# Performance work log

Measured on AMD Instinct MI355X. Metric: run time of the kernel, lower is better.

The kernel has to match this reference:

```python
import jax, jax.numpy as jnp
import numpy as np

UNITS = 20
EPS_GPE_STN = 0.1


def _w_lateral(units=UNITS, eps=EPS_GPE_STN):
    # Faithful port of generate_distance_matrix: grid_size = int(sqrt(units))
    grid_size = int(units ** 0.5)
    idx = np.arange(units)
    xi, yi = np.divmod(idx, grid_size)
    d = (xi[:, None] - xi[None, :]) ** 2 + (yi[:, None] - yi[None, :]) ** 2
    return jnp.asarray(np.exp(-d.astype(np.float32) / eps), dtype=jnp.float32)


def setup_inputs() -> dict:
    key = jax.random.key(0)
    ks = jax.random.split(key, 8)
    B = 524288
    k = 1.0 / np.sqrt(UNITS)  # PyTorch LSTMCell init scale
    x = jax.random.normal(ks[0], (B, UNITS), dtype=jnp.float32)
    h = jax.random.normal(ks[1], (B, UNITS), dtype=jnp.float32)
    c = jax.random.normal(ks[2], (B, UNITS), dtype=jnp.float32)
    W_ih = jax.random.uniform(ks[3], (4 * UNITS, UNITS), jnp.float32, -k, k)
    W_hh = jax.random.uniform(ks[4], (4 * UNITS, UNITS), jnp.float32, -k, k)
    b_ih = jax.random.uniform(ks[5], (4 * UNITS,), jnp.float32, -k, k)
    b_hh = jax.random.uniform(ks[6], (4 * UNITS,), jnp.float32, -k, k)
    W_lat = _w_lateral()
    return {"x": x, "h": h, "c": c, "W_ih": W_ih, "W_hh": W_hh,
            "b_ih": b_ih, "b_hh": b_hh, "W_lat": W_lat}


def reference(x, h, c, W_ih, W_hh, b_ih, b_hh, W_lat):
    # nn.LSTMCell: gates in (i, f, g, o) order
    gates = x @ W_ih.T + h @ W_hh.T + (b_ih + b_hh)  # [B, 4U]
    i, f, g, o = jnp.split(gates, 4, axis=-1)
    c_next = jax.nn.sigmoid(f) * c + jax.nn.sigmoid(i) * jnp.tanh(g)
    h_lstm = jax.nn.sigmoid(o) * jnp.tanh(c_next)
    # bmm(W_lateral, h[:, :, None]).squeeze(-1) == h @ W_lat.T, then tanh
    h_next = jnp.tanh(h_lstm @ W_lat.T)
    return (h_next, c_next)
```

## Files before the change

kernel.cpp:

```cpp
#include <hip/hip_runtime.h>

#define UNITS 20

typedef __attribute__((ext_vector_type(8))) short short8;
typedef __attribute__((ext_vector_type(4))) float floatx4;
typedef unsigned int u32;
typedef unsigned short u16;

__device__ __forceinline__ float rcpf_fast(float x) { return __builtin_amdgcn_rcpf(x); }
__device__ __forceinline__ float sigmoidf_fast(float x) { return rcpf_fast(1.0f + __expf(-x)); }
__device__ __forceinline__ float tanhf_fast(float x) { return 1.0f - 2.0f * rcpf_fast(1.0f + __expf(2.0f * x)); }

__device__ __forceinline__ u32 f2bf(float f) {
  u32 u = __builtin_bit_cast(u32, f);
  u += 0x7fffu + ((u >> 16) & 1u);
  return u >> 16;
}
__device__ __forceinline__ u32 pack2(float a, float b) { return f2bf(a) | (f2bf(b) << 16); }

__global__ void prep_kernel(const float* __restrict__ W_ih, const float* __restrict__ W_hh,
                            const float* __restrict__ b_ih, const float* __restrict__ b_hh,
                            const float* __restrict__ W_lat,
                            u16* __restrict__ fragsG, u16* __restrict__ fragsL,
                            float4* __restrict__ bias4) {
  int tid = threadIdx.x;
  for (int e = tid; e < 768; e += 256) {
    int fi = e >> 6, lane = e & 63;
    int r = lane & 15, q = lane >> 4;
    short8 v8;
    if (fi < 10) {
      int t = fi >> 1, cc = fi & 1;
      int gr = (r & 3) * 20 + (r >> 2) * 5 + t;
#pragma unroll
      for (int j = 0; j < 8; ++j) {
        int k = cc * 32 + q * 8 + j;
        float v = 0.0f;
        if (k < 20) v = W_ih[gr * UNITS + k];
        else if (k < 40) v = W_hh[gr * UNITS + (k - 20)];
        v8[j] = (short)f2bf(v);
      }
      *(short8*)(fragsG + (size_t)e * 8) = v8;
    } else {
      int t = fi - 10;
      int vr = t * 16 + r;
#pragma unroll
      for (int j = 0; j < 8; ++j) {
        int k = q * 8 + j;
        float v = (vr < 20 && k < 20) ? W_lat[vr * UNITS + k] : 0.0f;
        v8[j] = (short)f2bf(v);
      }
      *(short8*)(fragsL + (size_t)(t * 64 + lane) * 8) = v8;
    }
  }
  if (tid < 20)
    bias4[tid] = make_float4(b_ih[tid] + b_hh[tid],
                             b_ih[20 + tid] + b_hh[20 + tid],
                             b_ih[40 + tid] + b_hh[40 + tid],
                             b_ih[60 + tid] + b_hh[60 + tid]);
}

#define SZE 72
#define SHL 40

__global__ __launch_bounds__(256) void stn_main(
    const float* __restrict__ x, const float* __restrict__ h, const float* __restrict__ c,
    const u16* __restrict__ fragsG, const u16* __restrict__ fragsL,
    const float4* __restrict__ bias4, float* __restrict__ out, int B) {
  __shared__ unsigned char smem[19456];
  u16*   Zs = (u16*)smem;
  float* Cn = (float*)smem;
  float* Cs = (float*)(smem + 9216);
  float* Hn = (float*)(smem + 9216);
  u16*   Hl = (u16*)(smem + 14336);

  const int tid  = threadIdx.x;
  const int lane = tid & 63;
  const int wv   = tid >> 6;
  const int m = lane & 15, q = lane >> 4;
  const long rowBase = (long)blockIdx.x * 64;
  const int  myrow = wv * 16 + m;
  const long f4base = rowBase * 5;
  const long f4max = (long)B * 5 - 1;

  {
    const float4* x4 = (const float4*)x;
    const float4* h4 = (const float4*)h;
    const float4* c4 = (const float4*)c;
    for (int e = tid; e < 320; e += 256) {
      long gi = f4base + e; if (gi > f4max) gi = f4max;
      int row = e / 5, part = e - row * 5;
      float4 vx = x4[gi];
      u32* zp = (u32*)(Zs + row * SZE + part * 4);
      zp[0] = pack2(vx.x, vx.y); zp[1] = pack2(vx.z, vx.w);
      float4 vh = h4[gi];
      u32* zq = (u32*)(Zs + row * SZE + 20 + part * 4);
      zq[0] = pack2(vh.x, vh.y); zq[1] = pack2(vh.z, vh.w);
      ((float4*)Cs)[e] = c4[gi];
    }
    int r = tid & 63, s = tid >> 6;
    u32* zp = (u32*)(Zs + r * SZE + 40);
    zp[s * 3 + 0] = 0; zp[s * 3 + 1] = 0; zp[s * 3 + 2] = 0;
    u32* hp = (u32*)(Hl + r * SHL + 20);
    hp[s] = 0; if (s < 2) hp[s + 4] = 0;
  }
  __syncthreads();

  short8 bfr[2];
#pragma unroll
  for (int cc = 0; cc < 2; ++cc)
    bfr[cc] = *(const short8*)(Zs + myrow * SZE + cc * 32 + q * 8);

  floatx4 acc[5];
#pragma unroll
  for (int t = 0; t < 5; ++t) {
    float4 b4 = bias4[q * 5 + t];
    acc[t] = (floatx4){b4.x, b4.y, b4.z, b4.w};
#pragma unroll
    for (int cc = 0; cc < 2; ++cc) {
      short8 af = *(const short8*)(fragsG + (size_t)((t * 2 + cc) * 64 + lane) * 8);
      acc[t] = __builtin_amdgcn_mfma_f32_16x16x32_bf16(af, bfr[cc], acc[t], 0, 0, 0);
    }
  }

  float cnv[5];
#pragma unroll
  for (int t = 0; t < 5; ++t) {
    int u = q * 5 + t;
    float ig = sigmoidf_fast(acc[t][0]);
    float fg = sigmoidf_fast(acc[t][1]);
    float gg = tanhf_fast(acc[t][2]);
    float og = sigmoidf_fast(acc[t][3]);
    float cv = Cs[myrow * 20 + u];
    float cn = fg * cv + ig * gg;
    cnv[t] = cn;
    Hl[myrow * SHL + u] = (u16)f2bf(og * tanhf_fast(cn));
  }
  __syncthreads();

  short8 bl = *(const short8*)(Hl + myrow * SHL + q * 8);
  floatx4 accL[2];
#pragma unroll
  for (int t = 0; t < 2; ++t) {
    short8 al = *(const short8*)(fragsL + (size_t)(t * 64 + lane) * 8);
    accL[t] = __builtin_amdgcn_mfma_f32_16x16x32_bf16(al, bl, (floatx4){0.f, 0.f, 0.f, 0.f}, 0, 0, 0);
  }

#pragma unroll
  for (int t = 0; t < 5; ++t) Cn[myrow * 20 + q * 5 + t] = cnv[t];
#pragma unroll
  for (int t = 0; t < 2; ++t)
#pragma unroll
    for (int reg = 0; reg < 4; ++reg) {
      int v = t * 16 + q * 4 + reg;
      if (v < 20) Hn[myrow * 20 + v] = tanhf_fast(accL[t][reg]);
    }
  __syncthreads();

  {
    float4* outh4 = (float4*)out;
    float4* outc4 = (float4*)(out + (size_t)B * UNITS);
    for (int e = tid; e < 320; e += 256) {
      long gi = f4base + e;
      if (gi <= f4max) {
        outh4[gi] = ((const float4*)Hn)[e];
        outc4[gi] = ((const float4*)Cn)[e];
      }
    }
  }
}

extern "C" void kernel_launch(void* const* d_in, const int* in_sizes, int n_in,
                              void* d_out, int out_size, void* d_ws, size_t ws_size,
                              hipStream_t stream) {
  const float* x     = (const float*)d_in[0];
  const float* h     = (const float*)d_in[1];
  const float* c     = (const float*)d_in[2];
  const float* W_ih  = (const float*)d_in[3];
  const float* W_hh  = (const float*)d_in[4];
  const float* b_ih  = (const float*)d_in[5];
  const float* b_hh  = (const float*)d_in[6];
  const float* W_lat = (const float*)d_in[7];
  float* out = (float*)d_out;

  u16*    fragsG = (u16*)d_ws;
  u16*    fragsL = (u16*)((char*)d_ws + 10240);
  float4* bias4  = (float4*)((char*)d_ws + 12288);

  int B = in_sizes[0] / UNITS;
  prep_kernel<<<1, 256, 0, stream>>>(W_ih, W_hh, b_ih, b_hh, W_lat, fragsG, fragsL, bias4);
  int grid = (B + 63) / 64;
  stn_main<<<grid, 256, 0, stream>>>(x, h, c, fragsG, fragsL, bias4, out, B);
}
```

Measured before the change: 204.9 us.

## Load LSTM inputs straight into MFMA fragments with a persistent grid-stride loop

Removes the LDS staging of x, h and c and of the c_next and h_next outputs. Each lane now loads its own float4 pieces of x and h straight into the bf16 B-fragment layout, using the hardware v_cvt_pk_bf16_f32 packing. The lateral weight fragment is re-laid-out so that the LSTM output stays in registers and feeds the second MFMA without an LDS round trip. The grid is capped at 2048 blocks that loop over row chunks, and the gate weight fragments are cached once per block in LDS. The trade-off is less coalesced per-lane global loads and scalar stores for c in exchange for removing barriers and LDS traffic.

Result: no change. 205.1 us (+0.1%).

```diff
diff --git a/kernel.cpp b/kernel.cpp
--- a/kernel.cpp
+++ b/kernel.cpp
@@ -4,6 +4,7 @@
 
 typedef __attribute__((ext_vector_type(8))) short short8;
 typedef __attribute__((ext_vector_type(4))) float floatx4;
+typedef __attribute__((ext_vector_type(4))) unsigned int u32x4;
 typedef unsigned int u32;
 typedef unsigned short u16;
 
@@ -16,7 +17,11 @@
   u += 0x7fffu + ((u >> 16) & 1u);
   return u >> 16;
 }
-__device__ __forceinline__ u32 pack2(float a, float b) { return f2bf(a) | (f2bf(b) << 16); }
+__device__ __forceinline__ u32 cvtpk(float lo, float hi) {
+  u32 r;
+  asm("v_cvt_pk_bf16_f32 %0, %1, %2" : "=v"(r) : "v"(lo), "v"(hi));
+  return r;
+}
 
 __global__ void prep_kernel(const float* __restrict__ W_ih, const float* __restrict__ W_hh,
                             const float* __restrict__ b_ih, const float* __restrict__ b_hh,
@@ -45,8 +50,7 @@
       int vr = t * 16 + r;
 #pragma unroll
       for (int j = 0; j < 8; ++j) {
-        int k = q * 8 + j;
-        float v = (vr < 20 && k < 20) ? W_lat[vr * UNITS + k] : 0.0f;
+        float v = (vr < 20 && j < 5) ? W_lat[vr * UNITS + q * 5 + j] : 0.0f;
         v8[j] = (short)f2bf(v);
       }
       *(short8*)(fragsL + (size_t)(t * 64 + lane) * 8) = v8;
@@ -59,111 +63,103 @@
                              b_ih[60 + tid] + b_hh[60 + tid]);
 }
 
-#define SZE 72
-#define SHL 40
-
 __global__ __launch_bounds__(256) void stn_main(
     const float* __restrict__ x, const float* __restrict__ h, const float* __restrict__ c,
     const u16* __restrict__ fragsG, const u16* __restrict__ fragsL,
     const float4* __restrict__ bias4, float* __restrict__ out, int B) {
-  __shared__ unsigned char smem[19456];
-  u16*   Zs = (u16*)smem;
-  float* Cn = (float*)smem;
-  float* Cs = (float*)(smem + 9216);
-  float* Hn = (float*)(smem + 9216);
-  u16*   Hl = (u16*)(smem + 14336);
+  __shared__ float4 ldsGf[640];
+
+  {
+    const float4* src = (const float4*)fragsG;
+    for (int i = threadIdx.x; i < 640; i += 256) ldsGf[i] = src[i];
+  }
 
   const int tid  = threadIdx.x;
   const int lane = tid & 63;
   const int wv   = tid >> 6;
   const int m = lane & 15, q = lane >> 4;
-  const long rowBase = (long)blockIdx.x * 64;
-  const int  myrow = wv * 16 + m;
-  const long f4base = rowBase * 5;
-  const long f4max = (long)B * 5 - 1;
 
-  {
-    const float4* x4 = (const float4*)x;
-    const float4* h4 = (const float4*)h;
-    const float4* c4 = (const float4*)c;
-    for (int e = tid; e < 320; e += 256) {
-      long gi = f4base + e; if (gi > f4max) gi = f4max;
-      int row = e / 5, part = e - row * 5;
-      float4 vx = x4[gi];
-      u32* zp = (u32*)(Zs + row * SZE + part * 4);
-      zp[0] = pack2(vx.x, vx.y); zp[1] = pack2(vx.z, vx.w);
-      float4 vh = h4[gi];
-      u32* zq = (u32*)(Zs + row * SZE + 20 + part * 4);
-      zq[0] = pack2(vh.x, vh.y); zq[1] = pack2(vh.z, vh.w);
-      ((float4*)Cs)[e] = c4[gi];
-    }
-    int r = tid & 63, s = tid >> 6;
-    u32* zp = (u32*)(Zs + r * SZE + 40);
-    zp[s * 3 + 0] = 0; zp[s * 3 + 1] = 0; zp[s * 3 + 2] = 0;
-    u32* hp = (u32*)(Hl + r * SHL + 20);
-    hp[s] = 0; if (s < 2) hp[s + 4] = 0;
-  }
-  __syncthreads();
-
-  short8 bfr[2];
-#pragma unroll
-  for (int cc = 0; cc < 2; ++cc)
-    bfr[cc] = *(const short8*)(Zs + myrow * SZE + cc * 32 + q * 8);
-
-  floatx4 acc[5];
+  floatx4 biasr[5];
 #pragma unroll
   for (int t = 0; t < 5; ++t) {
     float4 b4 = bias4[q * 5 + t];
-    acc[t] = (floatx4){b4.x, b4.y, b4.z, b4.w};
-#pragma unroll
-    for (int cc = 0; cc < 2; ++cc) {
-      short8 af = *(const short8*)(fragsG + (size_t)((t * 2 + cc) * 64 + lane) * 8);
-      acc[t] = __builtin_amdgcn_mfma_f32_16x16x32_bf16(af, bfr[cc], acc[t], 0, 0, 0);
-    }
+    biasr[t] = (floatx4){b4.x, b4.y, b4.z, b4.w};
   }
+  short8 afL0 = *(const short8*)(fragsL + (size_t)(0 * 64 + lane) * 8);
+  short8 afL1 = *(const short8*)(fragsL + (size_t)(1 * 64 + lane) * 8);
 
-  float cnv[5];
-#pragma unroll
-  for (int t = 0; t < 5; ++t) {
-    int u = q * 5 + t;
-    float ig = sigmoidf_fast(acc[t][0]);
-    float fg = sigmoidf_fast(acc[t][1]);
-    float gg = tanhf_fast(acc[t][2]);
-    float og = sigmoidf_fast(acc[t][3]);
-    float cv = Cs[myrow * 20 + u];
-    float cn = fg * cv + ig * gg;
-    cnv[t] = cn;
-    Hl[myrow * SHL + u] = (u16)f2bf(og * tanhf_fast(cn));
-  }
   __syncthreads();
 
-  short8 bl = *(const short8*)(Hl + myrow * SHL + q * 8);
-  floatx4 accL[2];
+  const short8* aG = (const short8*)ldsGf;
+  const float4* x4 = (const float4*)x;
+  const float4* h4 = (const float4*)h;
+  float* outh = out;
+  float* outc = out + (size_t)B * UNITS;
+
+  const long stride = 64L * (long)gridDim.x;
+  for (long base = (long)blockIdx.x * 64; base < B; base += stride) {
+    long row = base + wv * 16 + m;
+    bool valid = row < (long)B;
+    long rl  = valid ? row : (long)B - 1;
+    long r5  = rl * 5;
+    long r20 = rl * 20;
+
+    float4 v0 = (q == 3) ? h4[r5 + 1] : x4[r5 + 2 * q];
+    float4 v1 = (q == 0) ? x4[r5 + 1]
+              : (q == 1) ? x4[r5 + 3]
+              : (q == 2) ? h4[r5 + 0] : h4[r5 + 2];
+    const float* cp = c + r20 + q * 5;
+    float cv0 = cp[0], cv1 = cp[1], cv2 = cp[2], cv3 = cp[3], cv4 = cp[4];
+    short8 bfr1 = {0, 0, 0, 0, 0, 0, 0, 0};
+    if (q == 0) {
+      float4 v2 = h4[r5 + 3];
+      float4 v3 = h4[r5 + 4];
+      u32x4 p1 = {cvtpk(v2.x, v2.y), cvtpk(v2.z, v2.w),
+                  cvtpk(v3.x, v3.y), cvtpk(v3.z, v3.w)};
+      bfr1 = __builtin_bit_cast(short8, p1);
+    }
+    u32x4 p0 = {cvtpk(v0.x, v0.y), cvtpk(v0.z, v0.w),
+                cvtpk(v1.x, v1.y), cvtpk(v1.z, v1.w)};
+    short8 bfr0 = __builtin_bit_cast(short8, p0);
+
+    floatx4 acc[5];
 #pragma unroll
-  for (int t = 0; t < 2; ++t) {
-    short8 al = *(const short8*)(fragsL + (size_t)(t * 64 + lane) * 8);
-    accL[t] = __builtin_amdgcn_mfma_f32_16x16x32_bf16(al, bl, (floatx4){0.f, 0.f, 0.f, 0.f}, 0, 0, 0);
-  }
+    for (int t = 0; t < 5; ++t) {
+      acc[t] = __builtin_amdgcn_mfma_f32_16x16x32_bf16(aG[(t * 2 + 0) * 64 + lane], bfr0, biasr[t], 0, 0, 0);
+      acc[t] = __builtin_amdgcn_mfma_f32_16x16x32_bf16(aG[(t * 2 + 1) * 64 + lane], bfr1, acc[t], 0, 0, 0);
+    }
 
+    float cvv[5] = {cv0, cv1, cv2, cv3, cv4};
+    float cn[5], hl[5];
 #pragma unroll
-  for (int t = 0; t < 5; ++t) Cn[myrow * 20 + q * 5 + t] = cnv[t];
-#pragma unroll
-  for (int t = 0; t < 2; ++t)
-#pragma unroll
-    for (int reg = 0; reg < 4; ++reg) {
-      int v = t * 16 + q * 4 + reg;
-      if (v < 20) Hn[myrow * 20 + v] = tanhf_fast(accL[t][reg]);
+    for (int t = 0; t < 5; ++t) {
+      float ig = sigmoidf_fast(acc[t][0]);
+      float fg = sigmoidf_fast(acc[t][1]);
+      float gg = tanhf_fast(acc[t][2]);
+      float og = sigmoidf_fast(acc[t][3]);
+      float cnv = fg * cvv[t] + ig * gg;
+      cn[t] = cnv;
+      hl[t] = og * tanhf_fast(cnv);
     }
-  __syncthreads();
 
-  {
-    float4* outh4 = (float4*)out;
-    float4* outc4 = (float4*)(out + (size_t)B * UNITS);
-    for (int e = tid; e < 320; e += 256) {
-      long gi = f4base + e;
-      if (gi <= f4max) {
-        outh4[gi] = ((const float4*)Hn)[e];
-        outc4[gi] = ((const float4*)Cn)[e];
+    u32x4 pl = {cvtpk(hl[0], hl[1]), cvtpk(hl[2], hl[3]), cvtpk(hl[4], 0.0f), 0u};
+    short8 bl = __builtin_bit_cast(short8, pl);
+    floatx4 z4 = {0.0f, 0.0f, 0.0f, 0.0f};
+    floatx4 accL0 = __builtin_amdgcn_mfma_f32_16x16x32_bf16(afL0, bl, z4, 0, 0, 0);
+    floatx4 accL1 = __builtin_amdgcn_mfma_f32_16x16x32_bf16(afL1, bl, z4, 0, 0, 0);
+
+    if (valid) {
+      float* co = outc + r20 + q * 5;
+      co[0] = cn[0]; co[1] = cn[1]; co[2] = cn[2]; co[3] = cn[3]; co[4] = cn[4];
+      float4 hv;
+      hv.x = tanhf_fast(accL0[0]); hv.y = tanhf_fast(accL0[1]);
+      hv.z = tanhf_fast(accL0[2]); hv.w = tanhf_fast(accL0[3]);
+      *(float4*)(outh + r20 + q * 4) = hv;
+      if (q == 0) {
+        float4 hw;
+        hw.x = tanhf_fast(accL1[0]); hw.y = tanhf_fast(accL1[1]);
+        hw.z = tanhf_fast(accL1[2]); hw.w = tanhf_fast(accL1[3]);
+        *(float4*)(outh + r20 + 16) = hw;
       }
     }
   }
@@ -188,6 +184,7 @@
 
   int B = in_sizes[0] / UNITS;
   prep_kernel<<<1, 256, 0, stream>>>(W_ih, W_hh, b_ih, b_hh, W_lat, fragsG, fragsL, bias4);
-  int grid = (B + 63) / 64;
+  long chunks = ((long)B + 63) / 64;
+  int grid = (int)(chunks < 2048 ? chunks : 2048);
   stn_main<<<grid, 256, 0, stream>>>(x, h, c, fragsG, fragsL, bias4, out, B);
 }
```
